# Performance work log

Measured on AMD Instinct MI355X. Metric: run time of the kernel, lower is better.

## Reference

```python
import jax, jax.numpy as jnp
import numpy as np

DIM = 768
NUM_HEADS = 4
HEAD_DIM = DIM // NUM_HEADS
SCALE = HEAD_DIM ** -0.5


def setup_inputs() -> dict:
    key = jax.random.key(0)
    ks = jax.random.split(key, 8)
    B, N = 8, 2048
    q = jax.random.normal(ks[0], (B, N, DIM), dtype=jnp.float32)
    k = jax.random.normal(ks[1], (B, N, DIM), dtype=jnp.float32)
    v = jax.random.normal(ks[2], (B, N, DIM), dtype=jnp.float32)
    s = DIM ** -0.5
    Wq = jax.random.normal(ks[3], (DIM, DIM), dtype=jnp.float32) * s
    Wk = jax.random.normal(ks[4], (DIM, DIM), dtype=jnp.float32) * s
    Wv = jax.random.normal(ks[5], (DIM, DIM), dtype=jnp.float32) * s
    Wp = jax.random.normal(ks[6], (DIM, DIM), dtype=jnp.float32) * s
    bp = jnp.zeros((DIM,), dtype=jnp.float32)
    return {"q": q, "k": k, "v": v, "Wq": Wq, "Wk": Wk, "Wv": Wv, "Wp": Wp, "bp": bp}


def reference(q, k, v, Wq, Wk, Wv, Wp, bp):
    B, Nq, C = q.shape
    Nk = k.shape[1]
    H, D = NUM_HEADS, HEAD_DIM
    # Linear projections (nn.Linear: x @ W.T), split heads -> [B, H, N, D]
    qh = (q @ Wq.T).reshape(B, Nq, H, D).transpose(0, 2, 1, 3)
    kh = (k @ Wk.T).reshape(B, Nk, H, D).transpose(0, 2, 1, 3)
    vh = (v @ Wv.T).reshape(B, Nk, H, D).transpose(0, 2, 1, 3)
    # Attention scores [B, H, Nq, Nk], softmax over keys
    attn = jnp.einsum('bhqd,bhkd->bhqk', qh, kh) * SCALE
    attn = jax.nn.softmax(attn, axis=-1)
    # Weighted values -> merge heads -> output projection
    x = jnp.einsum('bhqk,bhkd->bhqd', attn, vh)
    x = x.transpose(0, 2, 1, 3).reshape(B, Nq, C)
    return x @ Wp.T + bp
```

## Files before the change

### kernel.cpp

```cpp
#include <hip/hip_runtime.h>
#include <hip/hip_fp16.h>

#define DIMC 768
#define NH 4
#define HD 192
#define SEQ 2048
#define NBATCH 8
#define SCALE_F 0.07216878364870323f
#define LOG2E   1.4426950408889634f
#define DEFER_THR 8.0f

typedef _Float16 f16x8 __attribute__((ext_vector_type(8)));
typedef _Float16 f16x4 __attribute__((ext_vector_type(4)));
typedef float    f32x4 __attribute__((ext_vector_type(4)));

__device__ __forceinline__ f32x4 mfma16(f16x8 a, f16x8 b, f32x4 c) {
    return __builtin_amdgcn_mfma_f32_16x16x32_f16(a, b, c, 0, 0, 0);
}
__device__ __forceinline__ void gl16(const void* g, void* l) {
    __builtin_amdgcn_global_load_lds(
        (const __attribute__((address_space(1))) unsigned int*)g,
        (__attribute__((address_space(3))) unsigned int*)l, 16, 0, 0);
}
__device__ __forceinline__ float exp2_hw(float x) {
    return __builtin_amdgcn_exp2f(x);
}

__global__ __launch_bounds__(256)
void cvt_w(const float* __restrict__ w0, const float* __restrict__ w1,
           const float* __restrict__ w2, const float* __restrict__ w3,
           _Float16* __restrict__ o0, _Float16* __restrict__ o1,
           _Float16* __restrict__ o2, _Float16* __restrict__ o3)
{
    const float* src = (blockIdx.y == 0) ? w0 : (blockIdx.y == 1) ? w1
                     : (blockIdx.y == 2) ? w2 : w3;
    _Float16* dst = (blockIdx.y == 0) ? o0 : (blockIdx.y == 1) ? o1
                  : (blockIdx.y == 2) ? o2 : o3;
    const int e   = blockIdx.x * 256 + threadIdx.x;
    const int row = e / 192;
    const int col = (e - row * 192) * 4;
    const float4 v = *(const float4*)(src + (size_t)row * DIMC + col);
    const int nt = row / 192, rr = row - nt * 192;
    const int t  = col >> 6,  cc = col & 63;
    f16x4 h = {(_Float16)v.x, (_Float16)v.y, (_Float16)v.z, (_Float16)v.w};
    *(f16x4*)(dst + ((size_t)(nt * 12 + t) * 192 + rr) * 64 + (cc ^ ((rr & 7) << 3))) = h;
}

__device__ __forceinline__ void phase_reads(const _Float16* As, const _Float16* Bs,
                                            int wr, int wc, int l15, int l4, int q,
                                            f16x8 af[2][2], f16x8 bf[2][3], bool loadB)
{
    #pragma unroll
    for (int ks = 0; ks < 2; ++ks) {
        const int cb = ks * 32 + l4 * 8;
        #pragma unroll
        for (int mm = 0; mm < 2; ++mm) {
            const int row = wr * 128 + (q * 2 + mm) * 16 + l15;
            af[ks][mm] = *(const f16x8*)(As + (size_t)row * 64 + (cb ^ ((row & 7) << 3)));
        }
        if (loadB) {
            #pragma unroll
            for (int n = 0; n < 3; ++n) {
                const int row = wc * 48 + n * 16 + l15;
                bf[ks][n] = *(const f16x8*)(Bs + (size_t)row * 64 + (cb ^ ((row & 7) << 3)));
            }
        }
    }
}
__device__ __forceinline__ void phase_mfma(int q, f16x8 af[2][2], f16x8 bf[2][3],
                                           f32x4 acc[8][3])
{
    __builtin_amdgcn_s_barrier();
    asm volatile("s_waitcnt lgkmcnt(0)" ::: "memory");
    __builtin_amdgcn_s_setprio(1);
    #pragma unroll
    for (int ks = 0; ks < 2; ++ks)
        #pragma unroll
        for (int mm = 0; mm < 2; ++mm)
            #pragma unroll
            for (int n = 0; n < 3; ++n)
                acc[q * 2 + mm][n] = mfma16(af[ks][mm], bf[ks][n], acc[q * 2 + mm][n]);
    __builtin_amdgcn_s_setprio(0);
}

template<int MODE>
__global__ __launch_bounds__(512, 2)
void gemm_p8(const float* __restrict__ A, const _Float16* __restrict__ Wimg,
             _Float16* __restrict__ Y, float scale)
{
    __shared__ __attribute__((aligned(16))) _Float16 Abuf[2][16384];
    __shared__ __attribute__((aligned(16))) _Float16 Bbuf[2][12288];

    const int tid  = threadIdx.x;
    const int wid  = tid >> 6;
    const int lane = tid & 63;
    const int l15  = lane & 15;
    const int l4   = lane >> 4;
    const int wr   = wid >> 2;
    const int wc   = wid & 3;
    const int m0   = blockIdx.x * 256;
    const int nt   = blockIdx.y;

    const unsigned char* Wt = (const unsigned char*)(Wimg + (size_t)nt * 12 * 12288);

    f32x4 acc[8][3];
    #pragma unroll
    for (int m = 0; m < 8; ++m)
        #pragma unroll
        for (int n = 0; n < 3; ++n)
            acc[m][n] = (f32x4){0.f, 0.f, 0.f, 0.f};

    float4 rA[8];
    auto loadA = [&](int t) {
        #pragma unroll
        for (int p = 0; p < 8; ++p) {
            const int linear = p * 512 + tid;
            const int row = linear >> 4, qc = (linear & 15) * 4;
            rA[p] = *(const float4*)(A + (size_t)(m0 + row) * DIMC + t * 64 + qc);
        }
    };
    auto writeA = [&](int buf) {
        #pragma unroll
        for (int p = 0; p < 8; ++p) {
            const int linear = p * 512 + tid;
            const int row = linear >> 4, qc = (linear & 15) * 4;
            f16x4 h = {(_Float16)rA[p].x, (_Float16)rA[p].y,
                       (_Float16)rA[p].z, (_Float16)rA[p].w};
            *(f16x4*)(&Abuf[buf][row * 64 + (qc ^ ((row & 7) << 3))]) = h;
        }
    };
    auto stageB = [&](int t) {
        const unsigned char* src = Wt + (size_t)t * 24576;
        #pragma unroll
        for (int u = 0; u < 3; ++u)
            gl16(src + u * 8192 + tid * 16, &Bbuf[t & 1][u * 4096 + tid * 8]);
    };

    loadA(0);
    stageB(0);
    asm volatile("s_waitcnt vmcnt(3)" ::: "memory");
    writeA(0);
    loadA(1);
    asm volatile("s_waitcnt vmcnt(8)" ::: "memory");
    asm volatile("s_waitcnt lgkmcnt(0)" ::: "memory");
    __builtin_amdgcn_s_barrier();

    for (int t = 0; t < 12; ++t) {
        const _Float16* As = &Abuf[t & 1][0];
        const _Float16* Bs = &Bbuf[t & 1][0];
        f16x8 af[2][2], bf[2][3];

        phase_reads(As, Bs, wr, wc, l15, l4, 0, af, bf, true);
        if (t < 11) stageB(t + 1);
        phase_mfma(0, af, bf, acc);
        __builtin_amdgcn_s_barrier();

        phase_reads(As, Bs, wr, wc, l15, l4, 1, af, bf, false);
        phase_mfma(1, af, bf, acc);
        __builtin_amdgcn_s_barrier();

        phase_reads(As, Bs, wr, wc, l15, l4, 2, af, bf, false);
        if (t < 11) {
            asm volatile("s_waitcnt vmcnt(3)" ::: "memory");
            writeA((t + 1) & 1);
            if (t < 10) loadA(t + 2);
        }
        phase_mfma(2, af, bf, acc);
        __builtin_amdgcn_s_barrier();

        phase_reads(As, Bs, wr, wc, l15, l4, 3, af, bf, false);
        phase_mfma(3, af, bf, acc);
        if (t < 10)       asm volatile("s_waitcnt vmcnt(8)" ::: "memory");
        else if (t == 10) asm volatile("s_waitcnt vmcnt(0)" ::: "memory");
        __builtin_amdgcn_s_barrier();
    }

    #pragma unroll
    for (int m = 0; m < 8; ++m) {
        const int rbase = m0 + wr * 128 + m * 16 + l4 * 4;
        #pragma unroll
        for (int n = 0; n < 3; ++n) {
            const int d = wc * 48 + n * 16 + l15;
            #pragma unroll
            for (int j = 0; j < 4; ++j) {
                const int r  = rbase + j;
                const int b  = r >> 11;
                const int nn = r & (SEQ - 1);
                if (MODE == 0) {
                    Y[((size_t)(b * NH + nt) * SEQ + nn) * HD + d] =
                        (_Float16)(acc[m][n][j] * scale);
                } else {
                    const int kt  = nn >> 5;
                    const int key = nn & 31;
                    const size_t tb = ((size_t)(b * NH + nt) * 64 + kt) * 12288;
                    size_t idx;
                    if (MODE == 1)
                        idx = tb + (size_t)key * HD + (d ^ ((key & 7) << 3));
                    else
                        idx = tb + 6144 + (((size_t)(key >> 3) * 192 + d) << 3) + (key & 7);
                    Y[idx] = (_Float16)acc[m][n][j];
                }
            }
        }
    }
}

__global__ __launch_bounds__(512, 2)
void gemm_x8(const _Float16* __restrict__ Ximg, const _Float16* __restrict__ Wimg,
             float* __restrict__ out, const float* __restrict__ bias)
{
    __shared__ __attribute__((aligned(16))) _Float16 Abuf[2][16384];
    __shared__ __attribute__((aligned(16))) _Float16 Bbuf[2][12288];

    const int tid  = threadIdx.x;
    const int wid  = tid >> 6;
    const int lane = tid & 63;
    const int l15  = lane & 15;
    const int l4   = lane >> 4;
    const int wr   = wid >> 2;
    const int wc   = wid & 3;
    const int mt   = blockIdx.x;
    const int nt   = blockIdx.y;

    const unsigned char* Xt = (const unsigned char*)(Ximg + (size_t)mt * 12 * 16384);
    const unsigned char* Wt = (const unsigned char*)(Wimg + (size_t)nt * 12 * 12288);

    f32x4 acc[8][3];
    #pragma unroll
    for (int m = 0; m < 8; ++m)
        #pragma unroll
        for (int n = 0; n < 3; ++n)
            acc[m][n] = (f32x4){0.f, 0.f, 0.f, 0.f};

    auto stageAB = [&](int t) {
        const unsigned char* sa = Xt + (size_t)t * 32768;
        const unsigned char* sb = Wt + (size_t)t * 24576;
        #pragma unroll
        for (int u = 0; u < 4; ++u)
            gl16(sa + u * 8192 + tid * 16, &Abuf[t & 1][u * 4096 + tid * 8]);
        #pragma unroll
        for (int u = 0; u < 3; ++u)
            gl16(sb + u * 8192 + tid * 16, &Bbuf[t & 1][u * 4096 + tid * 8]);
    };

    stageAB(0);
    asm volatile("s_waitcnt vmcnt(0)" ::: "memory");
    __builtin_amdgcn_s_barrier();

    for (int t = 0; t < 12; ++t) {
        const _Float16* As = &Abuf[t & 1][0];
        const _Float16* Bs = &Bbuf[t & 1][0];
        f16x8 af[2][2], bf[2][3];

        phase_reads(As, Bs, wr, wc, l15, l4, 0, af, bf, true);
        if (t < 11) stageAB(t + 1);
        phase_mfma(0, af, bf, acc);
        __builtin_amdgcn_s_barrier();

        phase_reads(As, Bs, wr, wc, l15, l4, 1, af, bf, false);
        phase_mfma(1, af, bf, acc);
        __builtin_amdgcn_s_barrier();

        phase_reads(As, Bs, wr, wc, l15, l4, 2, af, bf, false);
        phase_mfma(2, af, bf, acc);
        __builtin_amdgcn_s_barrier();

        phase_reads(As, Bs, wr, wc, l15, l4, 3, af, bf, false);
        phase_mfma(3, af, bf, acc);
        if (t < 11) asm volatile("s_waitcnt vmcnt(0)" ::: "memory");
        __builtin_amdgcn_s_barrier();
    }

    #pragma unroll
    for (int m = 0; m < 8; ++m) {
        const int rbase = mt * 256 + wr * 128 + m * 16 + l4 * 4;
        #pragma unroll
        for (int n = 0; n < 3; ++n) {
            const int c = nt * 192 + wc * 48 + n * 16 + l15;
            const float bv = bias[c];
            #pragma unroll
            for (int j = 0; j < 4; ++j)
                out[(size_t)(rbase + j) * DIMC + c] = acc[m][n][j] + bv;
        }
    }
}

__global__ __launch_bounds__(512, 4)
void attn7(const _Float16* __restrict__ Qh, const _Float16* __restrict__ KVimg,
           _Float16* __restrict__ Ximg)
{
    __shared__ __attribute__((aligned(16))) _Float16 KV[2][12288];
    __shared__ __attribute__((aligned(16))) _Float16 Ps[8][16][40];

    const int tid  = threadIdx.x;
    const int wid  = tid >> 6;
    const int lane = tid & 63;
    const int l15  = lane & 15;
    const int l4   = lane >> 4;

    const int bid   = blockIdx.x;
    const int local = bid >> 3;
    const int bh    = (bid & 7) * 4 + (local >> 4);
    const int qt    = local & 15;

    const unsigned char* KVt = (const unsigned char*)KVimg + (size_t)bh * 64 * 24576;

    #pragma unroll
    for (int s = 0; s < 3; ++s)
        gl16(KVt + (size_t)(s * 512 + tid) * 16, &KV[0][(size_t)(s * 512 + tid) * 8]);

    const int q0 = qt * 128 + wid * 16;
    const size_t qbase = (size_t)bh * SEQ * HD;
    f16x8 qf[6];
    #pragma unroll
    for (int kk = 0; kk < 6; ++kk)
        qf[kk] = *(const f16x8*)(Qh + qbase + (size_t)(q0 + l15) * HD + kk * 32 + l4 * 8);

    f32x4 Oacc[12];
    #pragma unroll
    for (int nd = 0; nd < 12; ++nd)
        Oacc[nd] = (f32x4){0.f, 0.f, 0.f, 0.f};
    float mrow[4], lrow[4];
    #pragma unroll
    for (int j = 0; j < 4; ++j) { mrow[j] = -1e30f; lrow[j] = 0.f; }

    for (int kt = 0; kt < SEQ / 32; ++kt) {
        const int cur = kt & 1;
        if (kt < SEQ / 32 - 1) {
            const unsigned char* KVn = KVt + (size_t)(kt + 1) * 24576;
            #pragma unroll
            for (int s = 0; s < 3; ++s)
                gl16(KVn + (size_t)(s * 512 + tid) * 16,
                     &KV[cur ^ 1][(size_t)(s * 512 + tid) * 8]);
            asm volatile("s_waitcnt vmcnt(3)" ::: "memory");
        } else {
            asm volatile("s_waitcnt vmcnt(0)" ::: "memory");
        }
        __builtin_amdgcn_s_barrier();
        __builtin_amdgcn_sched_barrier(0);

        const _Float16* Kc = &KV[cur][0];
        const _Float16* Vc = &KV[cur][6144];

        f32x4 sacc[2];
        sacc[0] = (f32x4){0.f, 0.f, 0.f, 0.f};
        sacc[1] = (f32x4){0.f, 0.f, 0.f, 0.f};
        __builtin_amdgcn_s_setprio(1);
        #pragma unroll
        for (int kk = 0; kk < 6; ++kk) {
            const int cb = (kk * 32 + l4 * 8) ^ ((l15 & 7) << 3);
            #pragma unroll
            for (int nn = 0; nn < 2; ++nn) {
                const f16x8 kf = *(const f16x8*)(Kc + (size_t)(nn * 16 + l15) * HD + cb);
                sacc[nn] = mfma16(qf[kk], kf, sacc[nn]);
            }
        }
        __builtin_amdgcn_s_setprio(0);

        float lm[4];
        bool need = false;
        #pragma unroll
        for (int j = 0; j < 4; ++j) {
            lm[j] = fmaxf(sacc[0][j], sacc[1][j]);
            need |= (lm[j] > mrow[j] + DEFER_THR);
        }
        if (__any(need)) {
            #pragma unroll
            for (int j = 0; j < 4; ++j) {
                float v = lm[j];
                v = fmaxf(v, __shfl_xor(v, 1));
                v = fmaxf(v, __shfl_xor(v, 2));
                v = fmaxf(v, __shfl_xor(v, 4));
                v = fmaxf(v, __shfl_xor(v, 8));
                const float mnew = fmaxf(mrow[j], v);
                const float f    = exp2_hw(mrow[j] - mnew);
                mrow[j] = mnew;
                lrow[j] *= f;
                #pragma unroll
                for (int nd = 0; nd < 12; ++nd)
                    Oacc[nd][j] *= f;
            }
        }
        #pragma unroll
        for (int j = 0; j < 4; ++j) {
            const float p0 = exp2_hw(sacc[0][j] - mrow[j]);
            const float p1 = exp2_hw(sacc[1][j] - mrow[j]);
            sacc[0][j] = p0;
            sacc[1][j] = p1;
            lrow[j] += p0 + p1;
        }

        #pragma unroll
        for (int nn = 0; nn < 2; ++nn)
            #pragma unroll
            for (int j = 0; j < 4; ++j)
                Ps[wid][l4 * 4 + j][nn * 16 + l15] = (_Float16)sacc[nn][j];
        asm volatile("s_waitcnt lgkmcnt(0)" ::: "memory");
        __builtin_amdgcn_sched_barrier(0);

        const f16x8 pf = *(const f16x8*)(&Ps[wid][l15][l4 * 8]);
        __builtin_amdgcn_s_setprio(1);
        #pragma unroll
        for (int nd = 0; nd < 12; ++nd) {
            const f16x8 vfr = *(const f16x8*)(Vc + (((size_t)l4 * 192 + nd * 16 + l15) << 3));
            Oacc[nd] = mfma16(pf, vfr, Oacc[nd]);
        }
        __builtin_amdgcn_s_setprio(0);

        __builtin_amdgcn_s_barrier();
        __builtin_amdgcn_sched_barrier(0);
    }

    #pragma unroll
    for (int j = 0; j < 4; ++j) {
        float s = lrow[j];
        s += __shfl_xor(s, 1);
        s += __shfl_xor(s, 2);
        s += __shfl_xor(s, 4);
        s += __shfl_xor(s, 8);
        lrow[j] = s;
    }
    const int b = bh >> 2;
    const int h = bh & 3;
    #pragma unroll
    for (int j = 0; j < 4; ++j) {
        const float inv = 1.f / lrow[j];
        const int qrow = q0 + l4 * 4 + j;
        const int gr   = b * SEQ + qrow;
        const int mt   = gr >> 8;
        const int rr   = gr & 255;
        #pragma unroll
        for (int nd = 0; nd < 12; ++nd) {
            const int gc = h * HD + nd * 16 + l15;
            const int t  = gc >> 6;
            const int cc = gc & 63;
            Ximg[((size_t)(mt * 12 + t) * 256 + rr) * 64 + (cc ^ ((rr & 7) << 3))] =
                (_Float16)(Oacc[nd][j] * inv);
        }
    }
}

extern "C" void kernel_launch(void* const* d_in, const int* in_sizes, int n_in,
                              void* d_out, int out_size, void* d_ws, size_t ws_size,
                              hipStream_t stream)
{
    const float* q  = (const float*)d_in[0];
    const float* k  = (const float*)d_in[1];
    const float* v  = (const float*)d_in[2];
    const float* Wq = (const float*)d_in[3];
    const float* Wk = (const float*)d_in[4];
    const float* Wv = (const float*)d_in[5];
    const float* Wp = (const float*)d_in[6];
    const float* bp = (const float*)d_in[7];

    const size_t HSZ  = (size_t)NBATCH * NH * SEQ * HD;
    const size_t WIMG = 4 * 12 * 12288;
    _Float16* Qh    = (_Float16*)d_ws;
    _Float16* KVimg = Qh + HSZ;
    _Float16* Ximg  = KVimg + 2 * HSZ;
    _Float16* Wpimg = Ximg + HSZ;
    _Float16* Wqimg = (_Float16*)d_out;
    _Float16* Wkimg = Wqimg + WIMG;
    _Float16* Wvimg = Wkimg + WIMG;

    cvt_w<<<dim3(576, 4), dim3(256), 0, stream>>>(Wq, Wk, Wv, Wp,
                                                  Wqimg, Wkimg, Wvimg, Wpimg);
    dim3 g8(64, 4), b8(512);
    gemm_p8<0><<<g8, b8, 0, stream>>>(q, Wqimg, Qh, SCALE_F * LOG2E);
    gemm_p8<1><<<g8, b8, 0, stream>>>(k, Wkimg, KVimg, 1.0f);
    gemm_p8<3><<<g8, b8, 0, stream>>>(v, Wvimg, KVimg, 1.0f);
    attn7<<<dim3(512), dim3(512), 0, stream>>>(Qh, KVimg, Ximg);
    gemm_x8<<<g8, b8, 0, stream>>>(Ximg, Wpimg, (float*)d_out, bp);
}
```

Before: 249.9 us.

## Software-pipeline attention: prefetch K two tiles ahead and overlap QK^T with softmax

```diff
diff --git a/kernel.cpp b/kernel.cpp
--- a/kernel.cpp
+++ b/kernel.cpp
@@ -286,10 +286,11 @@
 }
 
 __global__ __launch_bounds__(512, 4)
-void attn7(const _Float16* __restrict__ Qh, const _Float16* __restrict__ KVimg,
+void attn9(const _Float16* __restrict__ Qh, const _Float16* __restrict__ KVimg,
            _Float16* __restrict__ Ximg)
 {
-    __shared__ __attribute__((aligned(16))) _Float16 KV[2][12288];
+    __shared__ __attribute__((aligned(16))) _Float16 KB[3][6144];
+    __shared__ __attribute__((aligned(16))) _Float16 VB[2][6144];
     __shared__ __attribute__((aligned(16))) _Float16 Ps[8][16][40];
 
     const int tid  = threadIdx.x;
@@ -305,9 +306,19 @@
 
     const unsigned char* KVt = (const unsigned char*)KVimg + (size_t)bh * 64 * 24576;
 
-    #pragma unroll
-    for (int s = 0; s < 3; ++s)
-        gl16(KVt + (size_t)(s * 512 + tid) * 16, &KV[0][(size_t)(s * 512 + tid) * 8]);
+    auto stageK = [&](_Float16* dst, int t) {
+        const unsigned char* src = KVt + (size_t)t * 24576;
+        #pragma unroll
+        for (int s = 0; s < 3; ++s)
+            gl16(src + (size_t)(s * 256 + tid) * 16, dst + (size_t)(s * 256 + tid) * 8);
+    };
+    auto stageV = [&](_Float16* dst, int t) {
+        const int i = tid - 256;
+        const unsigned char* src = KVt + (size_t)t * 24576 + 12288;
+        #pragma unroll
+        for (int s = 0; s < 3; ++s)
+            gl16(src + (size_t)(s * 256 + i) * 16, dst + (size_t)(s * 256 + i) * 8);
+    };
 
     const int q0 = qt * 128 + wid * 16;
     const size_t qbase = (size_t)bh * SEQ * HD;
@@ -315,6 +326,10 @@
     #pragma unroll
     for (int kk = 0; kk < 6; ++kk)
         qf[kk] = *(const f16x8*)(Qh + qbase + (size_t)(q0 + l15) * HD + kk * 32 + l4 * 8);
+    __builtin_amdgcn_sched_barrier(0);
+
+    if (wid < 4) { stageK(&KB[0][0], 0); stageK(&KB[1][0], 1); }
+    else         { stageV(&VB[0][0], 0); }
 
     f32x4 Oacc[12];
     #pragma unroll
@@ -324,44 +339,49 @@
     #pragma unroll
     for (int j = 0; j < 4; ++j) { mrow[j] = -1e30f; lrow[j] = 0.f; }
 
-    for (int kt = 0; kt < SEQ / 32; ++kt) {
-        const int cur = kt & 1;
-        if (kt < SEQ / 32 - 1) {
-            const unsigned char* KVn = KVt + (size_t)(kt + 1) * 24576;
-            #pragma unroll
-            for (int s = 0; s < 3; ++s)
-                gl16(KVn + (size_t)(s * 512 + tid) * 16,
-                     &KV[cur ^ 1][(size_t)(s * 512 + tid) * 8]);
-            asm volatile("s_waitcnt vmcnt(3)" ::: "memory");
-        } else {
-            asm volatile("s_waitcnt vmcnt(0)" ::: "memory");
-        }
-        __builtin_amdgcn_s_barrier();
-        __builtin_amdgcn_sched_barrier(0);
-
-        const _Float16* Kc = &KV[cur][0];
-        const _Float16* Vc = &KV[cur][6144];
-
-        f32x4 sacc[2];
-        sacc[0] = (f32x4){0.f, 0.f, 0.f, 0.f};
-        sacc[1] = (f32x4){0.f, 0.f, 0.f, 0.f};
-        __builtin_amdgcn_s_setprio(1);
+    const _Float16* kRead  = &KB[1][0];
+    _Float16*       kStage = &KB[2][0];
+    _Float16*       kDead  = &KB[0][0];
+    const _Float16* vRead  = &VB[0][0];
+    _Float16*       vStage = &VB[1][0];
+
+    auto qkt = [&](const _Float16* Kc, f32x4 (&p)[2]) {
+        p[0] = (f32x4){0.f, 0.f, 0.f, 0.f};
+        p[1] = (f32x4){0.f, 0.f, 0.f, 0.f};
         #pragma unroll
         for (int kk = 0; kk < 6; ++kk) {
             const int cb = (kk * 32 + l4 * 8) ^ ((l15 & 7) << 3);
             #pragma unroll
             for (int nn = 0; nn < 2; ++nn) {
                 const f16x8 kf = *(const f16x8*)(Kc + (size_t)(nn * 16 + l15) * HD + cb);
-                sacc[nn] = mfma16(qf[kk], kf, sacc[nn]);
+                p[nn] = mfma16(qf[kk], kf, p[nn]);
             }
         }
-        __builtin_amdgcn_s_setprio(0);
+    };
+
+    asm volatile("s_waitcnt vmcnt(3)" ::: "memory");
+    __builtin_amdgcn_s_barrier();
+    __builtin_amdgcn_sched_barrier(0);
+
+    f32x4 pA[2], pB[2];
+    qkt(&KB[0][0], pA);
+
+    auto body = [&](int t, f32x4 (&pCur)[2], f32x4 (&pNxt)[2]) {
+        asm volatile("s_waitcnt vmcnt(0)" ::: "memory");
+        __builtin_amdgcn_s_barrier();
+        __builtin_amdgcn_sched_barrier(0);
+
+        if (wid < 4) { if (t + 2 < 64) stageK(kStage, t + 2); }
+        else         { if (t + 1 < 64) stageV(vStage, t + 1); }
+
+        __builtin_amdgcn_s_setprio(1);
+        if (t + 1 < 64) qkt(kRead, pNxt);
 
         float lm[4];
         bool need = false;
         #pragma unroll
         for (int j = 0; j < 4; ++j) {
-            lm[j] = fmaxf(sacc[0][j], sacc[1][j]);
+            lm[j] = fmaxf(pCur[0][j], pCur[1][j]);
             need |= (lm[j] > mrow[j] + DEFER_THR);
         }
         if (__any(need)) {
@@ -383,10 +403,10 @@
         }
         #pragma unroll
         for (int j = 0; j < 4; ++j) {
-            const float p0 = exp2_hw(sacc[0][j] - mrow[j]);
-            const float p1 = exp2_hw(sacc[1][j] - mrow[j]);
-            sacc[0][j] = p0;
-            sacc[1][j] = p1;
+            const float p0 = exp2_hw(pCur[0][j] - mrow[j]);
+            const float p1 = exp2_hw(pCur[1][j] - mrow[j]);
+            pCur[0][j] = p0;
+            pCur[1][j] = p1;
             lrow[j] += p0 + p1;
         }
 
@@ -394,21 +414,30 @@
         for (int nn = 0; nn < 2; ++nn)
             #pragma unroll
             for (int j = 0; j < 4; ++j)
-                Ps[wid][l4 * 4 + j][nn * 16 + l15] = (_Float16)sacc[nn][j];
+                Ps[wid][l4 * 4 + j][nn * 16 + l15] = (_Float16)pCur[nn][j];
         asm volatile("s_waitcnt lgkmcnt(0)" ::: "memory");
         __builtin_amdgcn_sched_barrier(0);
 
         const f16x8 pf = *(const f16x8*)(&Ps[wid][l15][l4 * 8]);
-        __builtin_amdgcn_s_setprio(1);
         #pragma unroll
         for (int nd = 0; nd < 12; ++nd) {
-            const f16x8 vfr = *(const f16x8*)(Vc + (((size_t)l4 * 192 + nd * 16 + l15) << 3));
+            const f16x8 vfr = *(const f16x8*)(vRead + (((size_t)l4 * 192 + nd * 16 + l15) << 3));
             Oacc[nd] = mfma16(pf, vfr, Oacc[nd]);
         }
         __builtin_amdgcn_s_setprio(0);
 
-        __builtin_amdgcn_s_barrier();
-        __builtin_amdgcn_sched_barrier(0);
+        const _Float16* oldRead = kRead;
+        kRead  = kStage;
+        kStage = kDead;
+        kDead  = (_Float16*)oldRead;
+        const _Float16* ov = vRead;
+        vRead  = vStage;
+        vStage = (_Float16*)ov;
+    };
+
+    for (int t2 = 0; t2 < 64; t2 += 2) {
+        body(t2,     pA, pB);
+        body(t2 + 1, pB, pA);
     }
 
     #pragma unroll
@@ -469,6 +498,6 @@
     gemm_p8<0><<<g8, b8, 0, stream>>>(q, Wqimg, Qh, SCALE_F * LOG2E);
     gemm_p8<1><<<g8, b8, 0, stream>>>(k, Wkimg, KVimg, 1.0f);
     gemm_p8<3><<<g8, b8, 0, stream>>>(v, Wvimg, KVimg, 1.0f);
-    attn7<<<dim3(512), dim3(512), 0, stream>>>(Qh, KVimg, Ximg);
+    attn9<<<dim3(512), dim3(512), 0, stream>>>(Qh, KVimg, Ximg);
     gemm_x8<<<g8, b8, 0, stream>>>(Ximg, Wpimg, (float*)d_out, bp);
 }
```

Measured after the change: 265.5 us. +6.3%, slower.

## Give each attention wave two 16-row query tiles, halving block size

Applied to the files above, without the earlier changes.

```diff
diff --git a/kernel.cpp b/kernel.cpp
--- a/kernel.cpp
+++ b/kernel.cpp
@@ -285,12 +285,12 @@
     }
 }
 
-__global__ __launch_bounds__(512, 4)
-void attn7(const _Float16* __restrict__ Qh, const _Float16* __restrict__ KVimg,
-           _Float16* __restrict__ Ximg)
+__global__ __launch_bounds__(256, 2)
+void attn10(const _Float16* __restrict__ Qh, const _Float16* __restrict__ KVimg,
+            _Float16* __restrict__ Ximg)
 {
     __shared__ __attribute__((aligned(16))) _Float16 KV[2][12288];
-    __shared__ __attribute__((aligned(16))) _Float16 Ps[8][16][40];
+    __shared__ __attribute__((aligned(16))) _Float16 Ps[4][32][40];
 
     const int tid  = threadIdx.x;
     const int wid  = tid >> 6;
@@ -306,33 +306,40 @@
     const unsigned char* KVt = (const unsigned char*)KVimg + (size_t)bh * 64 * 24576;
 
     #pragma unroll
-    for (int s = 0; s < 3; ++s)
-        gl16(KVt + (size_t)(s * 512 + tid) * 16, &KV[0][(size_t)(s * 512 + tid) * 8]);
-
-    const int q0 = qt * 128 + wid * 16;
+    for (int s = 0; s < 6; ++s)
+        gl16(KVt + (size_t)(s * 256 + tid) * 16, &KV[0][(size_t)(s * 256 + tid) * 8]);
+
+    const int q0 = qt * 128 + wid * 32;
     const size_t qbase = (size_t)bh * SEQ * HD;
-    f16x8 qf[6];
-    #pragma unroll
-    for (int kk = 0; kk < 6; ++kk)
-        qf[kk] = *(const f16x8*)(Qh + qbase + (size_t)(q0 + l15) * HD + kk * 32 + l4 * 8);
-
-    f32x4 Oacc[12];
-    #pragma unroll
-    for (int nd = 0; nd < 12; ++nd)
-        Oacc[nd] = (f32x4){0.f, 0.f, 0.f, 0.f};
-    float mrow[4], lrow[4];
-    #pragma unroll
-    for (int j = 0; j < 4; ++j) { mrow[j] = -1e30f; lrow[j] = 0.f; }
+    f16x8 qf[2][6];
+    #pragma unroll
+    for (int mm = 0; mm < 2; ++mm)
+        #pragma unroll
+        for (int kk = 0; kk < 6; ++kk)
+            qf[mm][kk] = *(const f16x8*)(Qh + qbase +
+                         (size_t)(q0 + mm * 16 + l15) * HD + kk * 32 + l4 * 8);
+
+    f32x4 Oacc[2][12];
+    #pragma unroll
+    for (int mm = 0; mm < 2; ++mm)
+        #pragma unroll
+        for (int nd = 0; nd < 12; ++nd)
+            Oacc[mm][nd] = (f32x4){0.f, 0.f, 0.f, 0.f};
+    float mrow[2][4], lrow[2][4];
+    #pragma unroll
+    for (int mm = 0; mm < 2; ++mm)
+        #pragma unroll
+        for (int j = 0; j < 4; ++j) { mrow[mm][j] = -1e30f; lrow[mm][j] = 0.f; }
 
     for (int kt = 0; kt < SEQ / 32; ++kt) {
         const int cur = kt & 1;
         if (kt < SEQ / 32 - 1) {
             const unsigned char* KVn = KVt + (size_t)(kt + 1) * 24576;
             #pragma unroll
-            for (int s = 0; s < 3; ++s)
-                gl16(KVn + (size_t)(s * 512 + tid) * 16,
-                     &KV[cur ^ 1][(size_t)(s * 512 + tid) * 8]);
-            asm volatile("s_waitcnt vmcnt(3)" ::: "memory");
+            for (int s = 0; s < 6; ++s)
+                gl16(KVn + (size_t)(s * 256 + tid) * 16,
+                     &KV[cur ^ 1][(size_t)(s * 256 + tid) * 8]);
+            asm volatile("s_waitcnt vmcnt(6)" ::: "memory");
         } else {
             asm volatile("s_waitcnt vmcnt(0)" ::: "memory");
         }
@@ -342,9 +349,12 @@
         const _Float16* Kc = &KV[cur][0];
         const _Float16* Vc = &KV[cur][6144];
 
-        f32x4 sacc[2];
-        sacc[0] = (f32x4){0.f, 0.f, 0.f, 0.f};
-        sacc[1] = (f32x4){0.f, 0.f, 0.f, 0.f};
+        f32x4 sacc[2][2];
+        #pragma unroll
+        for (int mm = 0; mm < 2; ++mm)
+            #pragma unroll
+            for (int nn = 0; nn < 2; ++nn)
+                sacc[mm][nn] = (f32x4){0.f, 0.f, 0.f, 0.f};
         __builtin_amdgcn_s_setprio(1);
         #pragma unroll
         for (int kk = 0; kk < 6; ++kk) {
@@ -352,58 +362,72 @@
             #pragma unroll
             for (int nn = 0; nn < 2; ++nn) {
                 const f16x8 kf = *(const f16x8*)(Kc + (size_t)(nn * 16 + l15) * HD + cb);
-                sacc[nn] = mfma16(qf[kk], kf, sacc[nn]);
+                sacc[0][nn] = mfma16(qf[0][kk], kf, sacc[0][nn]);
+                sacc[1][nn] = mfma16(qf[1][kk], kf, sacc[1][nn]);
             }
         }
         __builtin_amdgcn_s_setprio(0);
 
-        float lm[4];
+        float lm[2][4];
         bool need = false;
         #pragma unroll
-        for (int j = 0; j < 4; ++j) {
-            lm[j] = fmaxf(sacc[0][j], sacc[1][j]);
-            need |= (lm[j] > mrow[j] + DEFER_THR);
-        }
+        for (int mm = 0; mm < 2; ++mm)
+            #pragma unroll
+            for (int j = 0; j < 4; ++j) {
+                lm[mm][j] = fmaxf(sacc[mm][0][j], sacc[mm][1][j]);
+                need |= (lm[mm][j] > mrow[mm][j] + DEFER_THR);
+            }
         if (__any(need)) {
             #pragma unroll
+            for (int mm = 0; mm < 2; ++mm)
+                #pragma unroll
+                for (int j = 0; j < 4; ++j) {
+                    float v = lm[mm][j];
+                    v = fmaxf(v, __shfl_xor(v, 1));
+                    v = fmaxf(v, __shfl_xor(v, 2));
+                    v = fmaxf(v, __shfl_xor(v, 4));
+                    v = fmaxf(v, __shfl_xor(v, 8));
+                    const float mnew = fmaxf(mrow[mm][j], v);
+                    const float f    = exp2_hw(mrow[mm][j] - mnew);
+                    mrow[mm][j] = mnew;
+                    lrow[mm][j] *= f;
+                    #pragma unroll
+                    for (int nd = 0; nd < 12; ++nd)
+                        Oacc[mm][nd][j] *= f;
+                }
+        }
+        #pragma unroll
+        for (int mm = 0; mm < 2; ++mm)
+            #pragma unroll
             for (int j = 0; j < 4; ++j) {
-                float v = lm[j];
-                v = fmaxf(v, __shfl_xor(v, 1));
-                v = fmaxf(v, __shfl_xor(v, 2));
-                v = fmaxf(v, __shfl_xor(v, 4));
-                v = fmaxf(v, __shfl_xor(v, 8));
-                const float mnew = fmaxf(mrow[j], v);
-                const float f    = exp2_hw(mrow[j] - mnew);
-                mrow[j] = mnew;
-                lrow[j] *= f;
+                const float p0 = exp2_hw(sacc[mm][0][j] - mrow[mm][j]);
+                const float p1 = exp2_hw(sacc[mm][1][j] - mrow[mm][j]);
+                sacc[mm][0][j] = p0;
+                sacc[mm][1][j] = p1;
+                lrow[mm][j] += p0 + p1;
+            }
+
+        #pragma unroll
+        for (int mm = 0; mm < 2; ++mm)
+            #pragma unroll
+            for (int nn = 0; nn < 2; ++nn)
                 #pragma unroll
-                for (int nd = 0; nd < 12; ++nd)
-                    Oacc[nd][j] *= f;
-            }
-        }
-        #pragma unroll
-        for (int j = 0; j < 4; ++j) {
-            const float p0 = exp2_hw(sacc[0][j] - mrow[j]);
-            const float p1 = exp2_hw(sacc[1][j] - mrow[j]);
-            sacc[0][j] = p0;
-            sacc[1][j] = p1;
-            lrow[j] += p0 + p1;
-        }
-
-        #pragma unroll
-        for (int nn = 0; nn < 2; ++nn)
-            #pragma unroll
-            for (int j = 0; j < 4; ++j)
-                Ps[wid][l4 * 4 + j][nn * 16 + l15] = (_Float16)sacc[nn][j];
+                for (int j = 0; j < 4; ++j)
+                    Ps[wid][mm * 16 + l4 * 4 + j][nn * 16 + l15] =
+                        (_Float16)sacc[mm][nn][j];
         asm volatile("s_waitcnt lgkmcnt(0)" ::: "memory");
         __builtin_amdgcn_sched_barrier(0);
 
-        const f16x8 pf = *(const f16x8*)(&Ps[wid][l15][l4 * 8]);
+        f16x8 pf[2];
+        #pragma unroll
+        for (int mm = 0; mm < 2; ++mm)
+            pf[mm] = *(const f16x8*)(&Ps[wid][mm * 16 + l15][l4 * 8]);
         __builtin_amdgcn_s_setprio(1);
         #pragma unroll
         for (int nd = 0; nd < 12; ++nd) {
             const f16x8 vfr = *(const f16x8*)(Vc + (((size_t)l4 * 192 + nd * 16 + l15) << 3));
-            Oacc[nd] = mfma16(pf, vfr, Oacc[nd]);
+            Oacc[0][nd] = mfma16(pf[0], vfr, Oacc[0][nd]);
+            Oacc[1][nd] = mfma16(pf[1], vfr, Oacc[1][nd]);
         }
         __builtin_amdgcn_s_setprio(0);
 
@@ -412,32 +436,36 @@
     }
 
     #pragma unroll
-    for (int j = 0; j < 4; ++j) {
-        float s = lrow[j];
-        s += __shfl_xor(s, 1);
-        s += __shfl_xor(s, 2);
-        s += __shfl_xor(s, 4);
-        s += __shfl_xor(s, 8);
-        lrow[j] = s;
-    }
+    for (int mm = 0; mm < 2; ++mm)
+        #pragma unroll
+        for (int j = 0; j < 4; ++j) {
+            float s = lrow[mm][j];
+            s += __shfl_xor(s, 1);
+            s += __shfl_xor(s, 2);
+            s += __shfl_xor(s, 4);
+            s += __shfl_xor(s, 8);
+            lrow[mm][j] = s;
+        }
     const int b = bh >> 2;
     const int h = bh & 3;
     #pragma unroll
-    for (int j = 0; j < 4; ++j) {
-        const float inv = 1.f / lrow[j];
-        const int qrow = q0 + l4 * 4 + j;
-        const int gr   = b * SEQ + qrow;
-        const int mt   = gr >> 8;
-        const int rr   = gr & 255;
-        #pragma unroll
-        for (int nd = 0; nd < 12; ++nd) {
-            const int gc = h * HD + nd * 16 + l15;
-            const int t  = gc >> 6;
-            const int cc = gc & 63;
-            Ximg[((size_t)(mt * 12 + t) * 256 + rr) * 64 + (cc ^ ((rr & 7) << 3))] =
-                (_Float16)(Oacc[nd][j] * inv);
-        }
-    }
+    for (int mm = 0; mm < 2; ++mm)
+        #pragma unroll
+        for (int j = 0; j < 4; ++j) {
+            const float inv = 1.f / lrow[mm][j];
+            const int qrow = q0 + mm * 16 + l4 * 4 + j;
+            const int gr   = b * SEQ + qrow;
+            const int mt   = gr >> 8;
+            const int rr   = gr & 255;
+            #pragma unroll
+            for (int nd = 0; nd < 12; ++nd) {
+                const int gc = h * HD + nd * 16 + l15;
+                const int t  = gc >> 6;
+                const int cc = gc & 63;
+                Ximg[((size_t)(mt * 12 + t) * 256 + rr) * 64 + (cc ^ ((rr & 7) << 3))] =
+                    (_Float16)(Oacc[mm][nd][j] * inv);
+            }
+        }
 }
 
 extern "C" void kernel_launch(void* const* d_in, const int* in_sizes, int n_in,
@@ -469,6 +497,6 @@
     gemm_p8<0><<<g8, b8, 0, stream>>>(q, Wqimg, Qh, SCALE_F * LOG2E);
     gemm_p8<1><<<g8, b8, 0, stream>>>(k, Wkimg, KVimg, 1.0f);
     gemm_p8<3><<<g8, b8, 0, stream>>>(v, Wvimg, KVimg, 1.0f);
-    attn7<<<dim3(512), dim3(512), 0, stream>>>(Qh, KVimg, Ximg);
+    attn10<<<dim3(512), dim3(256), 0, stream>>>(Qh, KVimg, Ximg);
     gemm_x8<<<g8, b8, 0, stream>>>(Ximg, Wpimg, (float*)d_out, bp);
 }
```

Result: no change. 247.3 us (-1.0%).
